# Kernel optimization log

Measured on AMD Instinct MI355X. Metric: run time of the kernel, lower is better.

The kernel has to match this reference:

```python
import jax, jax.numpy as jnp
import numpy as np

NEG = -1e8


def lstm_scan(x, lens, Wih, Whh, b):
    # x: [B,S,D], lens: [B] int. PyTorch gate order i,f,g,o. Returns [B,S,H], zero at pad.
    B, S, D = x.shape
    H = Whh.shape[1]
    xs = jnp.swapaxes(x, 0, 1)  # [S,B,D]
    ts = jnp.arange(S)

    def step(carry, inp):
        h, c = carry
        xt, t = inp
        gates = xt @ Wih.T + h @ Whh.T + b  # [B,4H]
        i, f, g, o = jnp.split(gates, 4, axis=-1)
        i, f, o = jax.nn.sigmoid(i), jax.nn.sigmoid(f), jax.nn.sigmoid(o)
        g = jnp.tanh(g)
        c_new = f * c + i * g
        h_new = o * jnp.tanh(c_new)
        valid = (t < lens)[:, None]
        h = jnp.where(valid, h_new, h)
        c = jnp.where(valid, c_new, c)
        out = jnp.where(valid, h_new, 0.0)
        return (h, c), out

    init = (jnp.zeros((B, H), x.dtype), jnp.zeros((B, H), x.dtype))
    _, outs = jax.lax.scan(step, init, (xs, ts))
    return jnp.swapaxes(outs, 0, 1)  # [B,S,H]


def bilstm(x, lens, Wih_f, Whh_f, b_f, Wih_b, Whh_b, b_b):
    # forward direction
    out_f = lstm_scan(x, lens, Wih_f, Whh_f, b_f)
    # backward: reverse the valid prefix per sample (packed-sequence semantics)
    S = x.shape[1]
    t = jnp.arange(S)[None, :]
    idx = jnp.where(t < lens[:, None], lens[:, None] - 1 - t, t)  # [B,S]
    xr = jnp.take_along_axis(x, idx[:, :, None], axis=1)
    out_r = lstm_scan(xr, lens, Wih_b, Whh_b, b_b)
    out_b = jnp.take_along_axis(out_r, idx[:, :, None], axis=1)
    return jnp.concatenate([out_f, out_b], axis=-1)


def tnet_forward(seqs_id, seqs_len, asps_len, asps_mask, sent_mask,
                 embed, Wih_f, Whh_f, b_f, Wih_b, Whh_b, b_b,
                 W_cpt, b_cpt, W_as, b_as, Wq, bq, Wk, bk, Wv, bv, Wd, bd):
    seqs = embed[seqs_id]                                   # [B,S,D] (dropout = eval identity)
    seqs_lstm = bilstm(seqs, seqs_len, Wih_f, Whh_f, b_f, Wih_b, Whh_b, b_b)  # [B,S,D]

    # ragged aspect gather + pad + mean == masked mean (asps_mask==0 marks aspect tokens)
    asp_sel = (asps_mask == 0).astype(seqs_lstm.dtype)       # [B,S]
    asps = (seqs_lstm * asp_sel[:, :, None]).sum(axis=1) / asps_len[:, None].astype(seqs_lstm.dtype)
    asps = asps[:, None, :]                                  # [B,1,D]

    # CPT layers (flag='AS'); Attentions = dot-product attn, out = softmax(QK^T + mask) @ K
    x = seqs_lstm
    for _ in range(2):
        score = jax.nn.softmax(jnp.einsum('bqd,bkd->bqk', x, seqs_lstm) + asps_mask[:, None, :], axis=-1)
        attn_out = jnp.einsum('bqk,bkd->bqd', score, seqs_lstm)
        combine = jnp.concatenate([attn_out, x], axis=-1)    # [B,S,2D]
        linear_out = jax.nn.relu(combine @ W_cpt.T + b_cpt)
        scale = jax.nn.sigmoid(x @ W_as.T + b_as)
        x = scale * linear_out + (1.0 - scale) * x

    # QKVAttention over sentence
    D = x.shape[-1]
    Qp = asps @ Wq.T + bq                                    # [B,1,D]
    Kp = x @ Wk.T + bk                                       # [B,S,D]
    Vp = x @ Wv.T + bv
    sc = jax.nn.softmax(jnp.einsum('bqd,bkd->bqk', Qp, Kp) / jnp.sqrt(jnp.asarray(D, x.dtype))
                        + sent_mask[:, None, :], axis=-1)    # [B,1,S]
    out = jnp.einsum('bqk,bkd->bqd', sc, Vp)                 # [B,1,D]
    logits = out[:, 0] @ Wd.T + bd                           # [B,n_class]
    return logits, sc[:, 0]


def setup_inputs() -> dict:
    B, S, V, D, H, NC = 64, 256, 30000, 512, 256, 3
    key = jax.random.key(0)
    ks = jax.random.split(key, 24)

    seqs_id = jax.random.randint(ks[0], (B, S), 0, V)
    seqs_len = jax.random.randint(ks[1], (B,), S // 2, S + 1)
    asps_len = jax.random.randint(ks[2], (B,), 1, 6)
    start = jax.random.randint(ks[3], (B,), 0, S // 2 - 8)   # aspect span inside valid prefix
    pos = jnp.arange(S)[None, :]
    in_span = (pos >= start[:, None]) & (pos < (start + asps_len)[:, None])
    asps_mask = jnp.where(in_span, 0.0, NEG).astype(jnp.float32)
    sent_mask = jnp.where(pos < seqs_len[:, None], 0.0, NEG).astype(jnp.float32)

    def nrm(k, shape, s=0.02):
        return (s * jax.random.normal(k, shape)).astype(jnp.float32)

    inp = dict(seqs_id=seqs_id, seqs_len=seqs_len, asps_len=asps_len,
               asps_mask=asps_mask, sent_mask=sent_mask,
               embed=nrm(ks[4], (V, D), 0.1),
               Wih_f=nrm(ks[5], (4 * H, D)), Whh_f=nrm(ks[6], (4 * H, H)), b_f=jnp.zeros((4 * H,), jnp.float32),
               Wih_b=nrm(ks[7], (4 * H, D)), Whh_b=nrm(ks[8], (4 * H, H)), b_b=jnp.zeros((4 * H,), jnp.float32),
               W_cpt=nrm(ks[9], (D, 2 * D)), b_cpt=jnp.zeros((D,), jnp.float32),
               W_as=nrm(ks[10], (D, D)), b_as=jnp.zeros((D,), jnp.float32),
               Wq=nrm(ks[11], (D, D)), bq=jnp.zeros((D,), jnp.float32),
               Wk=nrm(ks[12], (D, D)), bk=jnp.zeros((D,), jnp.float32),
               Wv=nrm(ks[13], (D, D)), bv=jnp.zeros((D,), jnp.float32),
               Wd=nrm(ks[14], (NC, D)), bd=jnp.zeros((NC,), jnp.float32))
    return inp


def reference(seqs_id, seqs_len, asps_len, asps_mask, sent_mask,
              embed, Wih_f, Whh_f, b_f, Wih_b, Whh_b, b_b,
              W_cpt, b_cpt, W_as, b_as, Wq, bq, Wk, bk, Wv, bv, Wd, bd):
    return tnet_forward(seqs_id, seqs_len, asps_len, asps_mask, sent_mask,
                        embed, Wih_f, Whh_f, b_f, Wih_b, Whh_b, b_b,
                        W_cpt, b_cpt, W_as, b_as, Wq, bq, Wk, bk, Wv, bv, Wd, bd)
```

## Files before the change

### kernel.cpp

```cpp
#include <hip/hip_runtime.h>
#include <math.h>

constexpr int B_ = 64, S_ = 256, D_ = 512, H_ = 256, NC_ = 3;
constexpr int BS = B_ * S_;
constexpr int G4 = 4 * H_;

typedef __attribute__((ext_vector_type(4))) float f32x4;
typedef __attribute__((ext_vector_type(8))) short s16x8;
typedef unsigned short u16;
typedef unsigned long long u64;

template<int ACT>
static __device__ __forceinline__ float activate(float v) {
  if constexpr (ACT == 1) return v > 0.f ? v : 0.f;
  else if constexpr (ACT == 2) return 1.f / (1.f + expf(-v));
  else return v;
}

static __device__ __forceinline__ u16 f2bf_rne(float f) {
  unsigned u = __float_as_uint(f);
  return (u16)((u + 0x7FFFu + ((u >> 16) & 1u)) >> 16);
}
static __device__ __forceinline__ float bf2f(u16 h) {
  return __uint_as_float(((unsigned)h) << 16);
}
static __device__ __forceinline__ void splitf(float f, u16& h, u16& l) {
  h = f2bf_rne(f);
  float r = f - bf2f(h);
  l = f2bf_rne(r);
}

__global__ __launch_bounds__(256) void split_w(
    const float* __restrict__ src, u16* __restrict__ h, u16* __restrict__ l, int n4)
{
  int i = blockIdx.x * 256 + threadIdx.x;
  if (i >= n4) return;
  float4 v = ((const float4*)src)[i];
  ushort4 hh, ll;
  splitf(v.x, hh.x, ll.x); splitf(v.y, hh.y, ll.y);
  splitf(v.z, hh.z, ll.z); splitf(v.w, hh.w, ll.w);
  ((ushort4*)h)[i] = hh;
  ((ushort4*)l)[i] = ll;
}

__global__ __launch_bounds__(256) void gather_split(
    const float* __restrict__ embed, const int* __restrict__ gidx,
    u16* __restrict__ h, u16* __restrict__ l)
{
  int i = blockIdx.x * 256 + threadIdx.x;
  if (i >= BS * D_ / 4) return;
  int r = i >> 7;
  int c = (i & 127) << 2;
  float4 v = *(const float4*)(embed + (size_t)gidx[r] * D_ + c);
  ushort4 hh, ll;
  splitf(v.x, hh.x, ll.x); splitf(v.y, hh.y, ll.y);
  splitf(v.z, hh.z, ll.z); splitf(v.w, hh.w, ll.w);
  ((ushort4*)h)[i] = hh;
  ((ushort4*)l)[i] = ll;
}

template<int ACT, bool BT, bool ADDC, bool ASPL, bool BSPL, bool OSPL>
__global__ __launch_bounds__(256) void mgemm(
    const float* __restrict__ Af, const u16* __restrict__ Ah, const u16* __restrict__ Al,
    const float* __restrict__ Bf, const u16* __restrict__ Bh, const u16* __restrict__ Bl,
    const float* __restrict__ bias, const float* __restrict__ Cin,
    float* __restrict__ Co, u16* __restrict__ Oh, u16* __restrict__ Ol,
    int M, int N, int K, int ldb, long sA, long sB, long sC)
{
  __shared__ u16 AH[128][40];
  __shared__ u16 AL[128][40];
  __shared__ u16 BH[128][40];
  __shared__ u16 BL[128][40];

  const int tid = threadIdx.x;
  const int w = tid >> 6, l = tid & 63;
  const int m0 = blockIdx.x * 128, n0 = blockIdx.y * 128;
  const long zA = (long)blockIdx.z * sA;
  const long zB = (long)blockIdx.z * sB;
  const long zC = (long)blockIdx.z * sC;

  f32x4 acc[2][8];
  #pragma unroll
  for (int i = 0; i < 2; ++i)
    #pragma unroll
    for (int j = 0; j < 8; ++j) acc[i][j] = (f32x4){0.f, 0.f, 0.f, 0.f};

  const int ar = tid >> 1, ahh = tid & 1;
  const int bk = tid >> 3, bnq = tid & 7;
  const int lr = l & 15, lk = (l >> 4) * 8;

  for (int kt = 0; kt < K; kt += 32) {
    {
      int m = m0 + ar;
      if constexpr (ASPL) {
        s16x8 h0 = (s16x8)0, h1 = (s16x8)0, l0 = (s16x8)0, l1 = (s16x8)0;
        if (m < M) {
          const u16* ph = Ah + zA + (size_t)m * K + kt + ahh * 16;
          const u16* pl = Al + zA + (size_t)m * K + kt + ahh * 16;
          h0 = *(const s16x8*)ph; h1 = *(const s16x8*)(ph + 8);
          l0 = *(const s16x8*)pl; l1 = *(const s16x8*)(pl + 8);
        }
        *(s16x8*)&AH[ar][ahh * 16] = h0; *(s16x8*)&AH[ar][ahh * 16 + 8] = h1;
        *(s16x8*)&AL[ar][ahh * 16] = l0; *(s16x8*)&AL[ar][ahh * 16 + 8] = l1;
      } else {
        float vv[16];
        if (m < M) {
          const float* pf = Af + zA + (size_t)m * K + kt + ahh * 16;
          #pragma unroll
          for (int c = 0; c < 4; ++c) {
            float4 v = ((const float4*)pf)[c];
            vv[c * 4] = v.x; vv[c * 4 + 1] = v.y; vv[c * 4 + 2] = v.z; vv[c * 4 + 3] = v.w;
          }
        } else {
          #pragma unroll
          for (int c = 0; c < 16; ++c) vv[c] = 0.f;
        }
        u16 hh[16], ll[16];
        #pragma unroll
        for (int c = 0; c < 16; ++c) splitf(vv[c], hh[c], ll[c]);
        *(s16x8*)&AH[ar][ahh * 16] = *(s16x8*)&hh[0];
        *(s16x8*)&AH[ar][ahh * 16 + 8] = *(s16x8*)&hh[8];
        *(s16x8*)&AL[ar][ahh * 16] = *(s16x8*)&ll[0];
        *(s16x8*)&AL[ar][ahh * 16 + 8] = *(s16x8*)&ll[8];
      }
    }
    if constexpr (BT) {
      if constexpr (BSPL) {
        const u16* ph = Bh + zB + (size_t)(n0 + ar) * ldb + kt + ahh * 16;
        const u16* pl = Bl + zB + (size_t)(n0 + ar) * ldb + kt + ahh * 16;
        *(s16x8*)&BH[ar][ahh * 16] = *(const s16x8*)ph;
        *(s16x8*)&BH[ar][ahh * 16 + 8] = *(const s16x8*)(ph + 8);
        *(s16x8*)&BL[ar][ahh * 16] = *(const s16x8*)pl;
        *(s16x8*)&BL[ar][ahh * 16 + 8] = *(const s16x8*)(pl + 8);
      } else {
        const float* pf = Bf + zB + (size_t)(n0 + ar) * ldb + kt + ahh * 16;
        float vv[16];
        #pragma unroll
        for (int c = 0; c < 4; ++c) {
          float4 v = ((const float4*)pf)[c];
          vv[c * 4] = v.x; vv[c * 4 + 1] = v.y; vv[c * 4 + 2] = v.z; vv[c * 4 + 3] = v.w;
        }
        u16 hh[16], ll[16];
        #pragma unroll
        for (int c = 0; c < 16; ++c) splitf(vv[c], hh[c], ll[c]);
        *(s16x8*)&BH[ar][ahh * 16] = *(s16x8*)&hh[0];
        *(s16x8*)&BH[ar][ahh * 16 + 8] = *(s16x8*)&hh[8];
        *(s16x8*)&BL[ar][ahh * 16] = *(s16x8*)&ll[0];
        *(s16x8*)&BL[ar][ahh * 16 + 8] = *(s16x8*)&ll[8];
      }
    } else {
      const u16* ph = Bh + zB + (size_t)(kt + bk) * ldb + n0 + bnq * 16;
      const u16* pl = Bl + zB + (size_t)(kt + bk) * ldb + n0 + bnq * 16;
      s16x8 h8a = *(const s16x8*)ph, h8b = *(const s16x8*)(ph + 8);
      s16x8 l8a = *(const s16x8*)pl, l8b = *(const s16x8*)(pl + 8);
      #pragma unroll
      for (int jj = 0; jj < 8; ++jj) {
        BH[bnq * 16 + jj][bk] = (u16)h8a[jj];
        BH[bnq * 16 + 8 + jj][bk] = (u16)h8b[jj];
        BL[bnq * 16 + jj][bk] = (u16)l8a[jj];
        BL[bnq * 16 + 8 + jj][bk] = (u16)l8b[jj];
      }
    }
    __syncthreads();

    s16x8 afh[2], afl[2];
    #pragma unroll
    for (int i = 0; i < 2; ++i) {
      afh[i] = *(const s16x8*)&AH[w * 32 + i * 16 + lr][lk];
      afl[i] = *(const s16x8*)&AL[w * 32 + i * 16 + lr][lk];
    }
    #pragma unroll
    for (int j = 0; j < 8; ++j) {
      s16x8 bfh = *(const s16x8*)&BH[j * 16 + lr][lk];
      s16x8 bfl = *(const s16x8*)&BL[j * 16 + lr][lk];
      #pragma unroll
      for (int i = 0; i < 2; ++i) {
        acc[i][j] = __builtin_amdgcn_mfma_f32_16x16x32_bf16(afl[i], bfh, acc[i][j], 0, 0, 0);
        acc[i][j] = __builtin_amdgcn_mfma_f32_16x16x32_bf16(afh[i], bfl, acc[i][j], 0, 0, 0);
        acc[i][j] = __builtin_amdgcn_mfma_f32_16x16x32_bf16(afh[i], bfh, acc[i][j], 0, 0, 0);
      }
    }
    __syncthreads();
  }

  const int rl = (l >> 4) * 4;
  #pragma unroll
  for (int j = 0; j < 8; ++j) {
    int n = n0 + j * 16 + lr;
    float bv = bias ? bias[n] : 0.f;
    #pragma unroll
    for (int i = 0; i < 2; ++i) {
      #pragma unroll
      for (int e = 0; e < 4; ++e) {
        int m = m0 + w * 32 + i * 16 + rl + e;
        if (m < M) {
          float v = acc[i][j][e] + bv;
          if constexpr (ADDC) v += Cin[zC + (size_t)m * N + n];
          v = activate<ACT>(v);
          if constexpr (OSPL) {
            u16 hh, ll; splitf(v, hh, ll);
            Oh[zC + (size_t)m * N + n] = hh;
            Ol[zC + (size_t)m * N + n] = ll;
          } else {
            Co[zC + (size_t)m * N + n] = v;
          }
        }
      }
    }
  }
}

__global__ __launch_bounds__(256) void wf_prep(
    const float* __restrict__ Wf, const float* __restrict__ Wb, u16* __restrict__ WF)
{
  int gid = blockIdx.x * 256 + threadIdx.x;
  int lane = gid & 63;
  int nt = (gid >> 6) & 1;
  int kt = (gid >> 7) & 7;
  int w  = (gid >> 10) & 3;
  int j  = (gid >> 12) & 7;
  int dir = gid >> 15;
  const float* W = dir ? Wb : Wf;
  int r = w * 256 + j * 32 + nt * 16 + (lane & 15);
  int kb = kt * 32 + (lane >> 4) * 8;
  const float* src = W + (size_t)r * H_ + kb;
  u16 hh[8], ll[8];
  #pragma unroll
  for (int c = 0; c < 2; ++c) {
    float4 v = ((const float4*)src)[c];
    splitf(v.x, hh[c*4+0], ll[c*4+0]); splitf(v.y, hh[c*4+1], ll[c*4+1]);
    splitf(v.z, hh[c*4+2], ll[c*4+2]); splitf(v.w, hh[c*4+3], ll[c*4+3]);
  }
  size_t off = (size_t)(gid >> 6) * 1024 + (size_t)lane * 8;
  *(s16x8*)(WF + off)       = *(s16x8*)&hh[0];
  *(s16x8*)(WF + off + 512) = *(s16x8*)&ll[0];
}

__global__ __launch_bounds__(256) void ring_init(u64* __restrict__ ring64)
{
  int i = blockIdx.x * 256 + threadIdx.x;
  __hip_atomic_store(&ring64[i], (u64)3, __ATOMIC_RELAXED, __HIP_MEMORY_SCOPE_AGENT);
}

__global__ __launch_bounds__(256, 1) void lstm_dist(
    const float* __restrict__ GX, const u16* __restrict__ WF,
    const int* __restrict__ lens, u16* __restrict__ outH, u16* __restrict__ outL,
    u64* __restrict__ ring64)
{
  const int bid = blockIdx.x;
  const int grp = bid & 7;
  const int j   = bid >> 3;
  const int dir = grp >> 2;
  const int bg  = grp & 3;
  const int b0g = bg * 16;
  const int tid = threadIdx.x;
  const int w = tid >> 6, l = tid & 63;

  const float* gx = GX + (size_t)dir * ((size_t)BS * G4);

  __shared__ int slen[16];
  __shared__ __align__(16) u16 AHs[16][264];
  __shared__ __align__(16) u16 ALs[16][264];
  __shared__ float act[2][4][16][33];
  if (tid < 16) slen[tid] = lens[b0g + tid];
  __syncthreads();

  s16x8 wh[8][2], wl[8][2];
  #pragma unroll
  for (int kt = 0; kt < 8; ++kt)
    #pragma unroll
    for (int nt = 0; nt < 2; ++nt) {
      size_t q = ((size_t)(((dir * 8 + j) * 4 + w) * 8 + kt) * 2 + nt);
      const u16* p = WF + q * 1024 + (size_t)l * 8;
      wh[kt][nt] = *(const s16x8*)p;
      wl[kt][nt] = *(const s16x8*)(p + 512);
    }

  const int ub = tid >> 4;
  const int uu = (tid & 15) * 2;
  const int len_b = slen[ub];
  float c0s = 0.f, c1s = 0.f, h0s = 0.f, h1s = 0.f;

  const int lr = l & 15, lkb = (l >> 4) * 8;

  for (int t = 0; t < S_; ++t) {
    float gxv[2][4];
    #pragma unroll
    for (int nt = 0; nt < 2; ++nt)
      #pragma unroll
      for (int e = 0; e < 4; ++e) {
        int b = (l >> 4) * 4 + e;
        int len = slen[b];
        int pos = dir ? (t < len ? len - 1 - t : t) : t;
        gxv[nt][e] = gx[(size_t)((b0g + b) * S_ + pos) * G4 + (w * 256 + j * 32 + nt * 16 + lr)];
      }

    f32x4 acc[2];
    acc[0] = (f32x4){0.f, 0.f, 0.f, 0.f};
    acc[1] = (f32x4){0.f, 0.f, 0.f, 0.f};

    if (t > 0) {
      const unsigned gen = (unsigned)(((t - 1) >> 2) & 3);
      const int slot = (t - 1) & 3;
      u64* rb = ring64 + ((size_t)slot * 8 + grp) * (16 * 128);
      u64 v[8];
      unsigned need = 0xFFu;
      do {
        unsigned nn = 0;
        #pragma unroll
        for (int k = 0; k < 8; ++k)
          if ((need >> k) & 1)
            v[k] = __hip_atomic_load(&rb[k * 256 + tid], __ATOMIC_RELAXED, __HIP_MEMORY_SCOPE_AGENT);
        #pragma unroll
        for (int k = 0; k < 8; ++k)
          if (((need >> k) & 1) && ((unsigned)v[k] & 3u) != gen) nn |= 1u << k;
        need = nn;
      } while (need);
      #pragma unroll
      for (int k = 0; k < 8; ++k) {
        int idx = k * 256 + tid;
        int b = idx >> 7, p = idx & 127;
        float f0 = __uint_as_float((unsigned)v[k] & ~3u);
        float f1 = __uint_as_float((unsigned)(v[k] >> 32));
        u16 hh0, ll0, hh1, ll1;
        splitf(f0, hh0, ll0); splitf(f1, hh1, ll1);
        *(unsigned*)&AHs[b][2 * p] = (unsigned)hh0 | ((unsigned)hh1 << 16);
        *(unsigned*)&ALs[b][2 * p] = (unsigned)ll0 | ((unsigned)ll1 << 16);
      }
      __syncthreads();
      #pragma unroll
      for (int kt = 0; kt < 8; ++kt) {
        s16x8 ah = *(const s16x8*)&AHs[lr][kt * 32 + lkb];
        s16x8 al = *(const s16x8*)&ALs[lr][kt * 32 + lkb];
        #pragma unroll
        for (int nt = 0; nt < 2; ++nt) {
          acc[nt] = __builtin_amdgcn_mfma_f32_16x16x32_bf16(al, wh[kt][nt], acc[nt], 0, 0, 0);
          acc[nt] = __builtin_amdgcn_mfma_f32_16x16x32_bf16(ah, wl[kt][nt], acc[nt], 0, 0, 0);
          acc[nt] = __builtin_amdgcn_mfma_f32_16x16x32_bf16(ah, wh[kt][nt], acc[nt], 0, 0, 0);
        }
      }
    }

    const int pb = t & 1;
    #pragma unroll
    for (int nt = 0; nt < 2; ++nt)
      #pragma unroll
      for (int e = 0; e < 4; ++e) {
        float v = acc[nt][e] + gxv[nt][e];
        v = (w == 2) ? tanhf(v) : 1.f / (1.f + expf(-v));
        act[pb][w][(l >> 4) * 4 + e][nt * 16 + lr] = v;
      }
    __syncthreads();

    {
      int pos = dir ? (t < len_b ? len_b - 1 - t : t) : t;
      bool valid = t < len_b;
      float i0 = act[pb][0][ub][uu],     f0 = act[pb][1][ub][uu],     g0 = act[pb][2][ub][uu],     o0 = act[pb][3][ub][uu];
      float i1 = act[pb][0][ub][uu + 1], f1 = act[pb][1][ub][uu + 1], g1 = act[pb][2][ub][uu + 1], o1 = act[pb][3][ub][uu + 1];
      float cn0 = fmaf(f0, c0s, i0 * g0), cn1 = fmaf(f1, c1s, i1 * g1);
      float hn0 = o0 * tanhf(cn0), hn1 = o1 * tanhf(cn1);
      if (valid) { c0s = cn0; h0s = hn0; c1s = cn1; h1s = hn1; }
      unsigned gen = (unsigned)((t >> 2) & 3);
      unsigned a0 = (__float_as_uint(h0s) & ~3u) | gen;
      unsigned a1 = __float_as_uint(h1s);
      u64 word = ((u64)a1 << 32) | (u64)a0;
      const int slot = t & 3;
      size_t ridx = ((size_t)slot * 8 + grp) * (16 * 128) + (size_t)ub * 128 + j * 16 + (tid & 15);
      __hip_atomic_store(&ring64[ridx], word, __ATOMIC_RELAXED, __HIP_MEMORY_SCOPE_AGENT);
      float ov0 = valid ? hn0 : 0.f, ov1 = valid ? hn1 : 0.f;
      u16 oh0, qq0, oh1, qq1;
      splitf(ov0, oh0, qq0); splitf(ov1, oh1, qq1);
      size_t obase = (size_t)((b0g + ub) * S_ + pos) * (2 * H_) + dir * H_ + j * 32 + uu;
      *(ushort2*)&outH[obase] = make_ushort2(oh0, oh1);
      *(ushort2*)&outL[obase] = make_ushort2(qq0, qq1);
    }
  }
}

__global__ __launch_bounds__(512) void asps_k(
    const u16* __restrict__ lh, const u16* __restrict__ ll,
    const float* __restrict__ amask, const int* __restrict__ alen, float* __restrict__ asps)
{
  int b = blockIdx.x, d = threadIdx.x;
  float acc = 0.f;
  for (int t = 0; t < S_; ++t)
    if (amask[b * S_ + t] == 0.f) {
      size_t i = ((size_t)(b * S_ + t)) * D_ + d;
      acc += bf2f(lh[i]) + bf2f(ll[i]);
    }
  asps[b * D_ + d] = acc / (float)alen[b];
}

__global__ __launch_bounds__(256) void softmax_rows(
    const float* __restrict__ p_, const float* __restrict__ mask,
    u16* __restrict__ ph, u16* __restrict__ pl)
{
  const int row = blockIdx.x;
  const int b = row >> 8;
  const int tid = threadIdx.x;
  const float* p = p_ + (size_t)row * S_;
  float v = p[tid] + mask[(b << 8) | tid];
  float m = v;
  #pragma unroll
  for (int off = 32; off > 0; off >>= 1) m = fmaxf(m, __shfl_xor(m, off));
  __shared__ float r1[4];
  __shared__ float r2[4];
  const int w = tid >> 6, l = tid & 63;
  if (l == 0) r1[w] = m;
  __syncthreads();
  m = fmaxf(fmaxf(r1[0], r1[1]), fmaxf(r1[2], r1[3]));
  float e = expf(v - m);
  float s = e;
  #pragma unroll
  for (int off = 32; off > 0; off >>= 1) s += __shfl_xor(s, off);
  if (l == 0) r2[w] = s;
  __syncthreads();
  s = r2[0] + r2[1] + r2[2] + r2[3];
  float o = e / s;
  u16 hh, ll; splitf(o, hh, ll);
  ph[(size_t)row * S_ + tid] = hh;
  pl[(size_t)row * S_ + tid] = ll;
}

__global__ __launch_bounds__(256) void xupdate(
    const u16* __restrict__ xh, const u16* __restrict__ xl,
    const float4* __restrict__ sc, const float4* __restrict__ lin,
    u16* __restrict__ oh, u16* __restrict__ ol, int n4)
{
  int i = blockIdx.x * 256 + threadIdx.x;
  if (i >= n4) return;
  ushort4 h4 = ((const ushort4*)xh)[i];
  ushort4 l4 = ((const ushort4*)xl)[i];
  float4 s = sc[i], lv = lin[i];
  float x0 = bf2f(h4.x) + bf2f(l4.x);
  float x1 = bf2f(h4.y) + bf2f(l4.y);
  float x2 = bf2f(h4.z) + bf2f(l4.z);
  float x3 = bf2f(h4.w) + bf2f(l4.w);
  float o0 = s.x * lv.x + (1.f - s.x) * x0;
  float o1 = s.y * lv.y + (1.f - s.y) * x1;
  float o2 = s.z * lv.z + (1.f - s.z) * x2;
  float o3 = s.w * lv.w + (1.f - s.w) * x3;
  ushort4 hh, ll;
  splitf(o0, hh.x, ll.x); splitf(o1, hh.y, ll.y);
  splitf(o2, hh.z, ll.z); splitf(o3, hh.w, ll.w);
  ((ushort4*)oh)[i] = hh;
  ((ushort4*)ol)[i] = ll;
}

__global__ __launch_bounds__(256) void final_sc_k(
    const float* __restrict__ Qp, const float* __restrict__ Kp,
    const float* __restrict__ smask, float* __restrict__ outsc)
{
  int b = blockIdx.x, tid = threadIdx.x;
  __shared__ float q[D_];
  q[tid] = Qp[b * D_ + tid];
  q[tid + 256] = Qp[b * D_ + tid + 256];
  __syncthreads();
  const float4* kr = (const float4*)(Kp + ((size_t)(b * S_ + tid)) * D_);
  float acc = 0.f;
  #pragma unroll 4
  for (int d = 0; d < D_ / 4; ++d) {
    float4 kv = kr[d];
    acc += q[4 * d] * kv.x + q[4 * d + 1] * kv.y + q[4 * d + 2] * kv.z + q[4 * d + 3] * kv.w;
  }
  float v = acc / sqrtf((float)D_) + smask[b * S_ + tid];
  float m = v;
  #pragma unroll
  for (int off = 32; off > 0; off >>= 1) m = fmaxf(m, __shfl_xor(m, off));
  __shared__ float r1[4];
  __shared__ float r2[4];
  const int w = tid >> 6, l = tid & 63;
  if (l == 0) r1[w] = m;
  __syncthreads();
  m = fmaxf(fmaxf(r1[0], r1[1]), fmaxf(r1[2], r1[3]));
  float e = expf(v - m);
  float s = e;
  #pragma unroll
  for (int off = 32; off > 0; off >>= 1) s += __shfl_xor(s, off);
  if (l == 0) r2[w] = s;
  __syncthreads();
  s = r2[0] + r2[1] + r2[2] + r2[3];
  outsc[b * S_ + tid] = e / s;
}

__global__ __launch_bounds__(512) void out_vec_k(
    const float* __restrict__ sc, const float* __restrict__ Vp, float* __restrict__ outv)
{
  int b = blockIdx.x, d = threadIdx.x;
  __shared__ float s[S_];
  if (d < S_) s[d] = sc[b * S_ + d];
  __syncthreads();
  float acc = 0.f;
  for (int k = 0; k < S_; ++k) acc = fmaf(s[k], Vp[((size_t)(b * S_ + k)) * D_ + d], acc);
  outv[b * D_ + d] = acc;
}

__global__ __launch_bounds__(192) void logits_k(
    const float* __restrict__ outv, const float* __restrict__ Wd,
    const float* __restrict__ bd, float* __restrict__ out)
{
  int b = blockIdx.x;
  int c = threadIdx.x >> 6, l = threadIdx.x & 63;
  float acc = 0.f;
  for (int d = l; d < D_; d += 64) acc = fmaf(outv[b * D_ + d], Wd[c * D_ + d], acc);
  #pragma unroll
  for (int off = 32; off > 0; off >>= 1) acc += __shfl_down(acc, off);
  if (l == 0) out[b * NC_ + c] = acc + bd[c];
}

extern "C" void kernel_launch(void* const* d_in, const int* in_sizes, int n_in,
                              void* d_out, int out_size, void* d_ws, size_t ws_size,
                              hipStream_t stream)
{
  const int*   seqs_id   = (const int*)d_in[0];
  const int*   seqs_len  = (const int*)d_in[1];
  const int*   asps_len  = (const int*)d_in[2];
  const float* asps_mask = (const float*)d_in[3];
  const float* sent_mask = (const float*)d_in[4];
  const float* embed     = (const float*)d_in[5];
  const float* Wih_f     = (const float*)d_in[6];
  const float* Whh_f     = (const float*)d_in[7];
  const float* b_f       = (const float*)d_in[8];
  const float* Wih_b     = (const float*)d_in[9];
  const float* Whh_b     = (const float*)d_in[10];
  const float* b_b       = (const float*)d_in[11];
  const float* W_cpt     = (const float*)d_in[12];
  const float* b_cpt     = (const float*)d_in[13];
  const float* W_as      = (const float*)d_in[14];
  const float* b_as      = (const float*)d_in[15];
  const float* Wq        = (const float*)d_in[16];
  const float* bq        = (const float*)d_in[17];
  const float* Wk        = (const float*)d_in[18];
  const float* bk        = (const float*)d_in[19];
  const float* Wv        = (const float*)d_in[20];
  const float* bv        = (const float*)d_in[21];
  const float* Wd        = (const float*)d_in[22];
  const float* bd        = (const float*)d_in[23];

  float* w = (float*)d_ws;
  size_t off = 0;
  auto alloc = [&](size_t words) { size_t o = off; off += words; return o; };
  struct Split { u16* h; u16* l; };
  auto salloc = [&](size_t n) {
    size_t o = alloc(n);
    Split s; s.h = (u16*)(w + o); s.l = (u16*)(w + o) + n; return s;
  };

  const size_t off_wf   = alloc(524288);
  const size_t off_ring = alloc(131072);
  Split sWihF = salloc(4ul * H_ * D_);
  Split sWihB = salloc(4ul * H_ * D_);
  Split sWcpt = salloc((size_t)D_ * 2 * D_);
  Split sWas  = salloc((size_t)D_ * D_);
  Split sWk   = salloc((size_t)D_ * D_);
  Split sWv   = salloc((size_t)D_ * D_);
  Split sWq   = salloc((size_t)D_ * D_);
  Split sLstm = salloc((size_t)BS * D_);
  const size_t off_asps = alloc((size_t)B_ * D_);
  const size_t off_qp   = alloc((size_t)B_ * D_);
  const size_t off_outv = alloc((size_t)B_ * D_);

  const size_t dyn0 = off;
  Split sXemb; sXemb.h = (u16*)(w + dyn0); sXemb.l = sXemb.h + (size_t)BS * D_;
  float* GX = w + dyn0 + (size_t)BS * D_;
  size_t p2 = dyn0;
  float* scoreF = w + p2;                 p2 += (size_t)B_ * S_ * S_;
  Split sScore; sScore.h = (u16*)(w + p2); sScore.l = sScore.h + (size_t)B_ * S_ * S_; p2 += (size_t)B_ * S_ * S_;
  Split sAttn;  sAttn.h  = (u16*)(w + p2); sAttn.l  = sAttn.h + (size_t)BS * D_;       p2 += (size_t)BS * D_;
  float* lin = w + p2;                    p2 += (size_t)BS * D_;
  float* scl = w + p2;                    p2 += (size_t)BS * D_;
  Split sX;     sX.h     = (u16*)(w + p2); sX.l     = sX.h + (size_t)BS * D_;           p2 += (size_t)BS * D_;

  u16* WF      = (u16*)(w + off_wf);
  u64* ring64  = (u64*)(w + off_ring);
  float* aspsb = w + off_asps;
  float* qp    = w + off_qp;
  float* outv  = w + off_outv;
  float* Kp    = (float*)sAttn.h;
  float* Vp    = lin;
  float* logits = (float*)d_out;
  float* outsc  = (float*)d_out + B_ * NC_;

  ring_init<<<256, 256, 0, stream>>>(ring64);
  wf_prep<<<256, 256, 0, stream>>>(Whh_f, Whh_b, WF);
  split_w<<<512, 256, 0, stream>>>(Wih_f, sWihF.h, sWihF.l, H_ * D_);
  split_w<<<512, 256, 0, stream>>>(Wih_b, sWihB.h, sWihB.l, H_ * D_);
  split_w<<<512, 256, 0, stream>>>(W_cpt, sWcpt.h, sWcpt.l, D_ * 2 * D_ / 4);
  split_w<<<256, 256, 0, stream>>>(W_as, sWas.h, sWas.l, D_ * D_ / 4);
  split_w<<<256, 256, 0, stream>>>(Wk, sWk.h, sWk.l, D_ * D_ / 4);
  split_w<<<256, 256, 0, stream>>>(Wv, sWv.h, sWv.l, D_ * D_ / 4);
  split_w<<<256, 256, 0, stream>>>(Wq, sWq.h, sWq.l, D_ * D_ / 4);
  gather_split<<<BS * D_ / 4 / 256, 256, 0, stream>>>(embed, seqs_id, sXemb.h, sXemb.l);

  mgemm<0, true, false, true, true, false><<<dim3(128, 8, 1), 256, 0, stream>>>(
      nullptr, sXemb.h, sXemb.l, nullptr, sWihF.h, sWihF.l, b_f, nullptr,
      GX, nullptr, nullptr, BS, G4, D_, D_, 0, 0, 0);
  mgemm<0, true, false, true, true, false><<<dim3(128, 8, 1), 256, 0, stream>>>(
      nullptr, sXemb.h, sXemb.l, nullptr, sWihB.h, sWihB.l, b_b, nullptr,
      GX + (size_t)BS * G4, nullptr, nullptr, BS, G4, D_, D_, 0, 0, 0);

  lstm_dist<<<64, 256, 0, stream>>>(GX, WF, seqs_len, sLstm.h, sLstm.l, ring64);
  asps_k<<<B_, D_, 0, stream>>>(sLstm.h, sLstm.l, asps_mask, asps_len, aspsb);

  for (int it = 0; it < 2; ++it) {
    const Split xin = (it == 0) ? sLstm : sX;
    mgemm<0, true, false, true, true, false><<<dim3(2, 2, B_), 256, 0, stream>>>(
        nullptr, xin.h, xin.l, nullptr, sLstm.h, sLstm.l, nullptr, nullptr,
        scoreF, nullptr, nullptr, S_, S_, D_, D_,
        (long)S_ * D_, (long)S_ * D_, (long)S_ * S_);
    softmax_rows<<<BS, 256, 0, stream>>>(scoreF, asps_mask, sScore.h, sScore.l);
    mgemm<0, false, false, true, true, true><<<dim3(2, 4, B_), 256, 0, stream>>>(
        nullptr, sScore.h, sScore.l, nullptr, sLstm.h, sLstm.l, nullptr, nullptr,
        nullptr, sAttn.h, sAttn.l, S_, D_, S_, D_,
        (long)S_ * S_, (long)S_ * D_, (long)S_ * D_);
    mgemm<0, true, false, true, true, false><<<dim3(128, 4, 1), 256, 0, stream>>>(
        nullptr, sAttn.h, sAttn.l, nullptr, sWcpt.h, sWcpt.l, b_cpt, nullptr,
        lin, nullptr, nullptr, BS, D_, D_, 2 * D_, 0, 0, 0);
    mgemm<1, true, true, true, true, false><<<dim3(128, 4, 1), 256, 0, stream>>>(
        nullptr, xin.h, xin.l, nullptr, sWcpt.h + D_, sWcpt.l + D_, nullptr, lin,
        lin, nullptr, nullptr, BS, D_, D_, 2 * D_, 0, 0, 0);
    mgemm<2, true, false, true, true, false><<<dim3(128, 4, 1), 256, 0, stream>>>(
        nullptr, xin.h, xin.l, nullptr, sWas.h, sWas.l, b_as, nullptr,
        scl, nullptr, nullptr, BS, D_, D_, D_, 0, 0, 0);
    xupdate<<<(BS * D_ / 4 + 255) / 256, 256, 0, stream>>>(
        xin.h, xin.l, (const float4*)scl, (const float4*)lin, sX.h, sX.l, BS * D_ / 4);
  }

  mgemm<0, true, false, true, true, false><<<dim3(128, 4, 1), 256, 0, stream>>>(
      nullptr, sX.h, sX.l, nullptr, sWk.h, sWk.l, bk, nullptr,
      Kp, nullptr, nullptr, BS, D_, D_, D_, 0, 0, 0);
  mgemm<0, true, false, true, true, false><<<dim3(128, 4, 1), 256, 0, stream>>>(
      nullptr, sX.h, sX.l, nullptr, sWv.h, sWv.l, bv, nullptr,
      Vp, nullptr, nullptr, BS, D_, D_, D_, 0, 0, 0);
  mgemm<0, true, false, false, true, false><<<dim3(1, 4, 1), 256, 0, stream>>>(
      aspsb, nullptr, nullptr, nullptr, sWq.h, sWq.l, bq, nullptr,
      qp, nullptr, nullptr, B_, D_, D_, D_, 0, 0, 0);

  final_sc_k<<<B_, 256, 0, stream>>>(qp, Kp, sent_mask, outsc);
  out_vec_k<<<B_, D_, 0, stream>>>(outsc, Vp, outv);
  logits_k<<<B_, 192, 0, stream>>>(outv, Wd, bd, logits);
}
```

Baseline: 1.587 ms.

## Run both LSTM directions per block and drop low-order recurrent weight split

```diff
diff --git a/kernel.cpp b/kernel.cpp
--- a/kernel.cpp
+++ b/kernel.cpp
@@ -224,16 +224,14 @@
   int r = w * 256 + j * 32 + nt * 16 + (lane & 15);
   int kb = kt * 32 + (lane >> 4) * 8;
   const float* src = W + (size_t)r * H_ + kb;
-  u16 hh[8], ll[8];
+  u16 hh[8];
   #pragma unroll
   for (int c = 0; c < 2; ++c) {
     float4 v = ((const float4*)src)[c];
-    splitf(v.x, hh[c*4+0], ll[c*4+0]); splitf(v.y, hh[c*4+1], ll[c*4+1]);
-    splitf(v.z, hh[c*4+2], ll[c*4+2]); splitf(v.w, hh[c*4+3], ll[c*4+3]);
+    hh[c*4+0] = f2bf_rne(v.x); hh[c*4+1] = f2bf_rne(v.y);
+    hh[c*4+2] = f2bf_rne(v.z); hh[c*4+3] = f2bf_rne(v.w);
   }
-  size_t off = (size_t)(gid >> 6) * 1024 + (size_t)lane * 8;
-  *(s16x8*)(WF + off)       = *(s16x8*)&hh[0];
-  *(s16x8*)(WF + off + 512) = *(s16x8*)&ll[0];
+  *(s16x8*)(WF + (size_t)(gid >> 6) * 512 + (size_t)lane * 8) = *(s16x8*)&hh[0];
 }
 
 __global__ __launch_bounds__(256) void ring_init(u64* __restrict__ ring64)
@@ -248,15 +246,11 @@
     u64* __restrict__ ring64)
 {
   const int bid = blockIdx.x;
-  const int grp = bid & 7;
-  const int j   = bid >> 3;
-  const int dir = grp >> 2;
-  const int bg  = grp & 3;
+  const int bg  = bid >> 3;
+  const int j   = bid & 7;
   const int b0g = bg * 16;
   const int tid = threadIdx.x;
   const int w = tid >> 6, l = tid & 63;
-
-  const float* gx = GX + (size_t)dir * ((size_t)BS * G4);
 
   __shared__ int slen[16];
   __shared__ __align__(16) u16 AHs[16][264];
@@ -265,114 +259,121 @@
   if (tid < 16) slen[tid] = lens[b0g + tid];
   __syncthreads();
 
-  s16x8 wh[8][2], wl[8][2];
-  #pragma unroll
-  for (int kt = 0; kt < 8; ++kt)
+  s16x8 wh[2][8][2];
+  #pragma unroll
+  for (int dir = 0; dir < 2; ++dir)
     #pragma unroll
-    for (int nt = 0; nt < 2; ++nt) {
-      size_t q = ((size_t)(((dir * 8 + j) * 4 + w) * 8 + kt) * 2 + nt);
-      const u16* p = WF + q * 1024 + (size_t)l * 8;
-      wh[kt][nt] = *(const s16x8*)p;
-      wl[kt][nt] = *(const s16x8*)(p + 512);
-    }
+    for (int kt = 0; kt < 8; ++kt)
+      #pragma unroll
+      for (int nt = 0; nt < 2; ++nt) {
+        size_t q = ((size_t)(((dir * 8 + j) * 4 + w) * 8 + kt) * 2 + nt);
+        wh[dir][kt][nt] = *(const s16x8*)(WF + q * 512 + (size_t)l * 8);
+      }
 
   const int ub = tid >> 4;
   const int uu = (tid & 15) * 2;
   const int len_b = slen[ub];
-  float c0s = 0.f, c1s = 0.f, h0s = 0.f, h1s = 0.f;
+  float cs0[2] = {0.f, 0.f}, hs0[2] = {0.f, 0.f};
+  float cs1[2] = {0.f, 0.f}, hs1[2] = {0.f, 0.f};
 
   const int lr = l & 15, lkb = (l >> 4) * 8;
 
   for (int t = 0; t < S_; ++t) {
-    float gxv[2][4];
     #pragma unroll
-    for (int nt = 0; nt < 2; ++nt)
+    for (int dir = 0; dir < 2; ++dir) {
+      const int grp = dir * 4 + bg;
+      const float* gx = GX + (size_t)dir * ((size_t)BS * G4);
+      float* cs = dir ? cs1 : cs0;
+      float* hs = dir ? hs1 : hs0;
+
+      float gxv[2][4];
       #pragma unroll
-      for (int e = 0; e < 4; ++e) {
-        int b = (l >> 4) * 4 + e;
-        int len = slen[b];
-        int pos = dir ? (t < len ? len - 1 - t : t) : t;
-        gxv[nt][e] = gx[(size_t)((b0g + b) * S_ + pos) * G4 + (w * 256 + j * 32 + nt * 16 + lr)];
-      }
-
-    f32x4 acc[2];
-    acc[0] = (f32x4){0.f, 0.f, 0.f, 0.f};
-    acc[1] = (f32x4){0.f, 0.f, 0.f, 0.f};
-
-    if (t > 0) {
-      const unsigned gen = (unsigned)(((t - 1) >> 2) & 3);
-      const int slot = (t - 1) & 3;
-      u64* rb = ring64 + ((size_t)slot * 8 + grp) * (16 * 128);
-      u64 v[8];
-      unsigned need = 0xFFu;
-      do {
-        unsigned nn = 0;
+      for (int nt = 0; nt < 2; ++nt)
         #pragma unroll
-        for (int k = 0; k < 8; ++k)
-          if ((need >> k) & 1)
-            v[k] = __hip_atomic_load(&rb[k * 256 + tid], __ATOMIC_RELAXED, __HIP_MEMORY_SCOPE_AGENT);
+        for (int e = 0; e < 4; ++e) {
+          int b = (l >> 4) * 4 + e;
+          int len = slen[b];
+          int pos = dir ? (t < len ? len - 1 - t : t) : t;
+          gxv[nt][e] = gx[(size_t)((b0g + b) * S_ + pos) * G4 + (w * 256 + j * 32 + nt * 16 + lr)];
+        }
+
+      f32x4 acc[2];
+      acc[0] = (f32x4){0.f, 0.f, 0.f, 0.f};
+      acc[1] = (f32x4){0.f, 0.f, 0.f, 0.f};
+
+      if (t > 0) {
+        const unsigned gen = (unsigned)(((t - 1) >> 2) & 3);
+        const int slot = (t - 1) & 3;
+        u64* rb = ring64 + ((size_t)slot * 8 + grp) * (16 * 128);
+        u64 v[8];
+        unsigned need = 0xFFu;
+        do {
+          unsigned nn = 0;
+          #pragma unroll
+          for (int k = 0; k < 8; ++k)
+            if ((need >> k) & 1)
+              v[k] = __hip_atomic_load(&rb[k * 256 + tid], __ATOMIC_RELAXED, __HIP_MEMORY_SCOPE_AGENT);
+          #pragma unroll
+          for (int k = 0; k < 8; ++k)
+            if (((need >> k) & 1) && ((unsigned)v[k] & 3u) != gen) nn |= 1u << k;
+          need = nn;
+        } while (need);
         #pragma unroll
-        for (int k = 0; k < 8; ++k)
-          if (((need >> k) & 1) && ((unsigned)v[k] & 3u) != gen) nn |= 1u << k;
-        need = nn;
-      } while (need);
+        for (int k = 0; k < 8; ++k) {
+          int idx = k * 256 + tid;
+          int b = idx >> 7, p = idx & 127;
+          float f0 = __uint_as_float((unsigned)v[k] & ~3u);
+          float f1 = __uint_as_float((unsigned)(v[k] >> 32));
+          u16 hh0, ll0, hh1, ll1;
+          splitf(f0, hh0, ll0); splitf(f1, hh1, ll1);
+          *(unsigned*)&AHs[b][2 * p] = (unsigned)hh0 | ((unsigned)hh1 << 16);
+          *(unsigned*)&ALs[b][2 * p] = (unsigned)ll0 | ((unsigned)ll1 << 16);
+        }
+        __syncthreads();
+        #pragma unroll
+        for (int kt = 0; kt < 8; ++kt) {
+          s16x8 ah = *(const s16x8*)&AHs[lr][kt * 32 + lkb];
+          s16x8 al = *(const s16x8*)&ALs[lr][kt * 32 + lkb];
+          #pragma unroll
+          for (int nt = 0; nt < 2; ++nt) {
+            acc[nt] = __builtin_amdgcn_mfma_f32_16x16x32_bf16(al, wh[dir][kt][nt], acc[nt], 0, 0, 0);
+            acc[nt] = __builtin_amdgcn_mfma_f32_16x16x32_bf16(ah, wh[dir][kt][nt], acc[nt], 0, 0, 0);
+          }
+        }
+      }
+
       #pragma unroll
-      for (int k = 0; k < 8; ++k) {
-        int idx = k * 256 + tid;
-        int b = idx >> 7, p = idx & 127;
-        float f0 = __uint_as_float((unsigned)v[k] & ~3u);
-        float f1 = __uint_as_float((unsigned)(v[k] >> 32));
-        u16 hh0, ll0, hh1, ll1;
-        splitf(f0, hh0, ll0); splitf(f1, hh1, ll1);
-        *(unsigned*)&AHs[b][2 * p] = (unsigned)hh0 | ((unsigned)hh1 << 16);
-        *(unsigned*)&ALs[b][2 * p] = (unsigned)ll0 | ((unsigned)ll1 << 16);
-      }
+      for (int nt = 0; nt < 2; ++nt)
+        #pragma unroll
+        for (int e = 0; e < 4; ++e) {
+          float vv = acc[nt][e] + gxv[nt][e];
+          vv = (w == 2) ? tanhf(vv) : 1.f / (1.f + expf(-vv));
+          act[dir][w][(l >> 4) * 4 + e][nt * 16 + lr] = vv;
+        }
       __syncthreads();
-      #pragma unroll
-      for (int kt = 0; kt < 8; ++kt) {
-        s16x8 ah = *(const s16x8*)&AHs[lr][kt * 32 + lkb];
-        s16x8 al = *(const s16x8*)&ALs[lr][kt * 32 + lkb];
-        #pragma unroll
-        for (int nt = 0; nt < 2; ++nt) {
-          acc[nt] = __builtin_amdgcn_mfma_f32_16x16x32_bf16(al, wh[kt][nt], acc[nt], 0, 0, 0);
-          acc[nt] = __builtin_amdgcn_mfma_f32_16x16x32_bf16(ah, wl[kt][nt], acc[nt], 0, 0, 0);
-          acc[nt] = __builtin_amdgcn_mfma_f32_16x16x32_bf16(ah, wh[kt][nt], acc[nt], 0, 0, 0);
-        }
-      }
-    }
-
-    const int pb = t & 1;
-    #pragma unroll
-    for (int nt = 0; nt < 2; ++nt)
-      #pragma unroll
-      for (int e = 0; e < 4; ++e) {
-        float v = acc[nt][e] + gxv[nt][e];
-        v = (w == 2) ? tanhf(v) : 1.f / (1.f + expf(-v));
-        act[pb][w][(l >> 4) * 4 + e][nt * 16 + lr] = v;
-      }
-    __syncthreads();
-
-    {
-      int pos = dir ? (t < len_b ? len_b - 1 - t : t) : t;
-      bool valid = t < len_b;
-      float i0 = act[pb][0][ub][uu],     f0 = act[pb][1][ub][uu],     g0 = act[pb][2][ub][uu],     o0 = act[pb][3][ub][uu];
-      float i1 = act[pb][0][ub][uu + 1], f1 = act[pb][1][ub][uu + 1], g1 = act[pb][2][ub][uu + 1], o1 = act[pb][3][ub][uu + 1];
-      float cn0 = fmaf(f0, c0s, i0 * g0), cn1 = fmaf(f1, c1s, i1 * g1);
-      float hn0 = o0 * tanhf(cn0), hn1 = o1 * tanhf(cn1);
-      if (valid) { c0s = cn0; h0s = hn0; c1s = cn1; h1s = hn1; }
-      unsigned gen = (unsigned)((t >> 2) & 3);
-      unsigned a0 = (__float_as_uint(h0s) & ~3u) | gen;
-      unsigned a1 = __float_as_uint(h1s);
-      u64 word = ((u64)a1 << 32) | (u64)a0;
-      const int slot = t & 3;
-      size_t ridx = ((size_t)slot * 8 + grp) * (16 * 128) + (size_t)ub * 128 + j * 16 + (tid & 15);
-      __hip_atomic_store(&ring64[ridx], word, __ATOMIC_RELAXED, __HIP_MEMORY_SCOPE_AGENT);
-      float ov0 = valid ? hn0 : 0.f, ov1 = valid ? hn1 : 0.f;
-      u16 oh0, qq0, oh1, qq1;
-      splitf(ov0, oh0, qq0); splitf(ov1, oh1, qq1);
-      size_t obase = (size_t)((b0g + ub) * S_ + pos) * (2 * H_) + dir * H_ + j * 32 + uu;
-      *(ushort2*)&outH[obase] = make_ushort2(oh0, oh1);
-      *(ushort2*)&outL[obase] = make_ushort2(qq0, qq1);
+
+      {
+        int pos = dir ? (t < len_b ? len_b - 1 - t : t) : t;
+        bool valid = t < len_b;
+        float i0 = act[dir][0][ub][uu],     f0 = act[dir][1][ub][uu],     g0 = act[dir][2][ub][uu],     o0 = act[dir][3][ub][uu];
+        float i1 = act[dir][0][ub][uu + 1], f1 = act[dir][1][ub][uu + 1], g1 = act[dir][2][ub][uu + 1], o1 = act[dir][3][ub][uu + 1];
+        float cn0 = fmaf(f0, cs[0], i0 * g0), cn1 = fmaf(f1, cs[1], i1 * g1);
+        float hn0 = o0 * tanhf(cn0), hn1 = o1 * tanhf(cn1);
+        if (valid) { cs[0] = cn0; hs[0] = hn0; cs[1] = cn1; hs[1] = hn1; }
+        unsigned gen = (unsigned)((t >> 2) & 3);
+        unsigned a0 = (__float_as_uint(hs[0]) & ~3u) | gen;
+        unsigned a1 = __float_as_uint(hs[1]);
+        u64 word = ((u64)a1 << 32) | (u64)a0;
+        const int slot = t & 3;
+        size_t ridx = ((size_t)slot * 8 + grp) * (16 * 128) + (size_t)ub * 128 + j * 16 + (tid & 15);
+        __hip_atomic_store(&ring64[ridx], word, __ATOMIC_RELAXED, __HIP_MEMORY_SCOPE_AGENT);
+        float ov0 = valid ? hn0 : 0.f, ov1 = valid ? hn1 : 0.f;
+        u16 oh0, qq0, oh1, qq1;
+        splitf(ov0, oh0, qq0); splitf(ov1, oh1, qq1);
+        size_t obase = (size_t)((b0g + ub) * S_ + pos) * (2 * H_) + dir * H_ + j * 32 + uu;
+        *(ushort2*)&outH[obase] = make_ushort2(oh0, oh1);
+        *(ushort2*)&outL[obase] = make_ushort2(qq0, qq1);
+      }
     }
   }
 }
@@ -546,7 +547,7 @@
     Split s; s.h = (u16*)(w + o); s.l = (u16*)(w + o) + n; return s;
   };
 
-  const size_t off_wf   = alloc(524288);
+  const size_t off_wf   = alloc(262144);
   const size_t off_ring = alloc(131072);
   Split sWihF = salloc(4ul * H_ * D_);
   Split sWihB = salloc(4ul * H_ * D_);
@@ -599,7 +600,7 @@
       nullptr, sXemb.h, sXemb.l, nullptr, sWihB.h, sWihB.l, b_b, nullptr,
       GX + (size_t)BS * G4, nullptr, nullptr, BS, G4, D_, D_, 0, 0, 0);
 
-  lstm_dist<<<64, 256, 0, stream>>>(GX, WF, seqs_len, sLstm.h, sLstm.l, ring64);
+  lstm_dist<<<32, 256, 0, stream>>>(GX, WF, seqs_len, sLstm.h, sLstm.l, ring64);
   asps_k<<<B_, D_, 0, stream>>>(sLstm.h, sLstm.l, asps_mask, asps_len, aspsb);
 
   for (int it = 0; it < 2; ++it) {
```

Result: slower. 2.179 ms (+37.3%).
